# Kernel optimization log

Measured on AMD Instinct MI355X. Metric: run time of the kernel, lower is better.

The kernel has to match this reference:

```python
import jax, jax.numpy as jnp
import numpy as np

B, N, E = 16, 2048, 1024
G, V = 2, 320
D = E // G
TAU = 2.0


def setup_inputs() -> dict:
    key = jax.random.key(0)
    k1, k2, k3, k4 = jax.random.split(key, 4)
    x = jax.random.normal(k1, (B, N, E), dtype=jnp.float32)
    u = jax.random.uniform(k2, (B, N, G, V), dtype=jnp.float32)
    W = jax.random.normal(k3, (E, G * V), dtype=jnp.float32) * 0.02
    b = jnp.zeros((G * V,), dtype=jnp.float32)
    codebook = jax.random.normal(k4, (G, V, D), dtype=jnp.float32)
    return {"x": x, "u": u, "W": W, "b": b, "codebook": codebook}


def reference(x, u, W, b, codebook):
    Bx, Nx, Ex = x.shape
    Gx, Vx, Dx = codebook.shape
    # linear projection -> per-group logits [B,N,G,V]
    h = (jnp.einsum('bne,ef->bnf', x, W) + b).reshape(Bx, Nx, Gx, Vx)
    # gumbel noise from uniform samples (clamped away from 0/1)
    eps = 1e-7
    g = -jnp.log(-jnp.log(u * (1.0 - 2.0 * eps) + eps))
    soft = jax.nn.softmax((h + g) / TAU, axis=-1)
    # hard one-hot with straight-through estimator (matches torch hard=True)
    idx = jnp.argmax(soft, axis=-1)
    hard = jax.nn.one_hot(idx, Vx, dtype=soft.dtype)
    y = hard - jax.lax.stop_gradient(soft) + soft  # [B,N,G,V]
    # select code vectors: equivalent to broadcast-mul + sum over V
    code_vector = jnp.einsum('bngv,gvd->bngd', y, codebook).reshape(Bx, Nx, Gx * Dx)
    # codebook usage entropy: sum one-hots over time, softmax over V per group
    p = jax.nn.softmax(jnp.sum(y, axis=1), axis=-1)  # [B,G,V]
    entropy = -jnp.sum(p * jnp.log(p + 1e-8)) / (Gx * Vx)
    return code_vector, entropy
```

## Files before the change

kernel.cpp:

```cpp
#include <hip/hip_runtime.h>

namespace {

constexpr int Bsz = 16, Nsz = 2048, Esz = 1024, Gsz = 2, Vsz = 320, Dsz = 512;
constexpr int Msz = Bsz * Nsz;
constexpr int Fsz = Gsz * Vsz;
constexpr int BM = 128, BN = 128, BK = 32;
constexpr int NKC = Esz / 32;
constexpr int NMB = Msz / 16;
constexpr int NFB = Fsz / 16;

typedef __attribute__((ext_vector_type(8))) short bf16x8;
typedef __attribute__((ext_vector_type(4))) float f32x4;
typedef unsigned int u32;
typedef unsigned short u16;

__device__ __forceinline__ void load_lds16(const void* g, void* l) {
  __builtin_amdgcn_global_load_lds(
      (const __attribute__((address_space(1))) u32*)g,
      (__attribute__((address_space(3))) u32*)l, 16, 0, 0);
}

__device__ __forceinline__ ushort f2bf(float f) {
  union { float f; unsigned u; } v; v.f = f;
  unsigned r = (v.u + 0x7FFFu + ((v.u >> 16) & 1u)) >> 16;
  return (ushort)r;
}
__device__ __forceinline__ float bf2f(ushort h) {
  union { unsigned u; float f; } v; v.u = ((unsigned)h) << 16;
  return v.f;
}

__device__ __forceinline__ float gumb_precise(float uu) {
  const float C0 = 1.0f - 2.0f * 1e-7f;
  float up = uu * C0;
  up = up + 1e-7f;
  return -logf(-logf(up));
}
__device__ __forceinline__ float gumb_fast(float uu) {
  const float C0 = 1.0f - 2.0f * 1e-7f;
  const float up = fmaf(uu, C0, 1e-7f);
  const float d = 1.0f - up;
  const float ypoly =
      d * fmaf(d, fmaf(d, fmaf(d, fmaf(d, 0.2f, 0.25f), 0.33333334f), 0.5f), 1.0f);
  const float yfast = -__logf(up);
  const float y = (up >= 0.84f) ? ypoly : yfast;
  return -__logf(y);
}

struct Top2 { float v1, v2; int i1, i2; };
__device__ __forceinline__ void t2_feed(Top2& t, float z, int f) {
  if (z > t.v1 || (z == t.v1 && f < t.i1)) {
    t.v2 = t.v1; t.i2 = t.i1; t.v1 = z; t.i1 = f;
  } else if (z > t.v2 || (z == t.v2 && f < t.i2)) {
    t.v2 = z; t.i2 = f;
  }
}
__device__ __forceinline__ void t2_merge(Top2& t, float ov1, int oi1, float ov2,
                                         int oi2) {
  if (ov1 > t.v1 || (ov1 == t.v1 && oi1 < t.i1)) {
    const bool keep = (t.v1 > ov2) || (t.v1 == ov2 && t.i1 < oi2);
    t.v2 = keep ? t.v1 : ov2; t.i2 = keep ? t.i1 : oi2;
    t.v1 = ov1; t.i1 = oi1;
  } else if (ov1 > t.v2 || (ov1 == t.v2 && oi1 < t.i2)) {
    t.v2 = ov1; t.i2 = oi1;
  }
}

__device__ __forceinline__ uint2 pack_hi_trunc(float4 a) {
  uint2 r;
  r.x = (__float_as_uint(a.x) >> 16) | (__float_as_uint(a.y) & 0xffff0000u);
  r.y = (__float_as_uint(a.z) >> 16) | (__float_as_uint(a.w) & 0xffff0000u);
  return r;
}
__device__ __forceinline__ float4 resid_trunc(float4 a) {
  float4 r;
  r.x = a.x - __uint_as_float(__float_as_uint(a.x) & 0xffff0000u);
  r.y = a.y - __uint_as_float(__float_as_uint(a.y) & 0xffff0000u);
  r.z = a.z - __uint_as_float(__float_as_uint(a.z) & 0xffff0000u);
  r.w = a.w - __uint_as_float(__float_as_uint(a.w) & 0xffff0000u);
  return r;
}


__global__ __launch_bounds__(256) void k_prep(const float* __restrict__ W,
                                              u16* __restrict__ wt,
                                              float* __restrict__ wtT) {
  const int tid = threadIdx.x;
  const int l = tid & 63;
  const int blob = blockIdx.x * 4 + (tid >> 6);
  const int fb = blob >> 5, kc = blob & 31;
  const int f = fb * 16 + (l & 15);
  const int k0 = kc * 32 + (l >> 4) * 8;
  float v[8];
  ushort hh[8], ll[8];
#pragma unroll
  for (int j = 0; j < 8; ++j) {
    v[j] = W[(size_t)(k0 + j) * Fsz + f];
    hh[j] = f2bf(v[j]);
    ll[j] = f2bf(v[j] - bf2f(hh[j]));
  }
  uint4 qh, ql;
  qh.x = hh[0] | ((u32)hh[1] << 16); qh.y = hh[2] | ((u32)hh[3] << 16);
  qh.z = hh[4] | ((u32)hh[5] << 16); qh.w = hh[6] | ((u32)hh[7] << 16);
  ql.x = ll[0] | ((u32)ll[1] << 16); ql.y = ll[2] | ((u32)ll[3] << 16);
  ql.z = ll[4] | ((u32)ll[5] << 16); ql.w = ll[6] | ((u32)ll[7] << 16);
  const size_t b2 = (size_t)(kc * NFB + fb);
  *(uint4*)(wt + (b2 * 2 + 0) * 512 + l * 8) = qh;
  *(uint4*)(wt + (b2 * 2 + 1) * 512 + l * 8) = ql;
  float4 t0, t1;
  t0.x = v[0]; t0.y = v[1]; t0.z = v[2]; t0.w = v[3];
  t1.x = v[4]; t1.y = v[5]; t1.z = v[6]; t1.w = v[7];
  *(float4*)(wtT + (size_t)f * Esz + k0) = t0;
  *(float4*)(wtT + (size_t)f * Esz + k0 + 4) = t1;
}

__global__ __launch_bounds__(256) void k_prepx(const float* __restrict__ x,
                                               u16* __restrict__ xt) {
  const int tid = threadIdx.x;
  const int l = tid & 63;
  const int blob = blockIdx.x * 4 + (tid >> 6);
  const int mb = blob >> 5, kc = blob & 31;
  const size_t row = (size_t)mb * 16 + (l & 15);
  const int k0 = kc * 32 + (l >> 4) * 8;
  const float4 a0 = *(const float4*)(x + row * Esz + k0);
  const float4 a1 = *(const float4*)(x + row * Esz + k0 + 4);
  const uint2 h0 = pack_hi_trunc(a0), h1 = pack_hi_trunc(a1);
  const uint2 l0 = pack_hi_trunc(resid_trunc(a0));
  const uint2 l1 = pack_hi_trunc(resid_trunc(a1));
  uint4 qh, ql;
  qh.x = h0.x; qh.y = h0.y; qh.z = h1.x; qh.w = h1.y;
  ql.x = l0.x; ql.y = l0.y; ql.z = l1.x; ql.w = l1.y;
  const size_t b2 = (size_t)kc * NMB + mb;
  *(uint4*)(xt + (b2 * 2 + 0) * 512 + l * 8) = qh;
  *(uint4*)(xt + (b2 * 2 + 1) * 512 + l * 8) = ql;
}

__global__ __launch_bounds__(256, 4) void k_gemm(
    const float* __restrict__ u, const float* __restrict__ bias,
    const u16* __restrict__ xt, const u16* __restrict__ wt,
    float4* __restrict__ partial) {
  __shared__ __align__(16) u16 sm[8192];

  const int tid = threadIdx.x;
  const int bid = blockIdx.x;
  const int tile = (bid & 7) * 320 + (bid >> 3);
  const int mt = tile / 10, nt = tile - mt * 10;
  const int m0 = mt * BM;
  const int n0 = nt * 64;

  const int lane = tid & 63, w = tid >> 6;
  const int lrow = lane & 15, quad = lane >> 4;

  f32x4 acc[2][4];
#pragma unroll
  for (int i = 0; i < 2; ++i)
#pragma unroll
    for (int j = 0; j < 4; ++j) acc[i][j] = (f32x4){0.f, 0.f, 0.f, 0.f};

  const size_t KSTEP_A = (size_t)NMB * 1024;
  const size_t KSTEP_B = (size_t)NFB * 1024;
  const u16* abase = xt + (size_t)(m0 >> 4) * 1024 + lane * 8;
  const u16* wbase = wt + (size_t)(n0 >> 4) * 1024 + lane * 8;

  auto stageA = [&](int kc) {
    const u16* s = abase + (size_t)kc * KSTEP_A;
#pragma unroll
    for (int i = 0; i < 4; ++i) {
      const int cc = w + 4 * i;
      load_lds16(s + cc * 512, sm + cc * 512);
    }
  };

  bf16x8 bh[4], bl[4];
  auto loadB = [&](int kc) {
    const u16* s = wbase + (size_t)kc * KSTEP_B;
#pragma unroll
    for (int ct = 0; ct < 4; ++ct) {
      bh[ct] = *(const bf16x8*)(s + ct * 1024);
      bl[ct] = *(const bf16x8*)(s + ct * 1024 + 512);
    }
  };

  stageA(0);
  loadB(0);

  for (int kc = 0; kc < NKC; ++kc) {
    __syncthreads();
    bf16x8 ah[2], al[2];
#pragma unroll
    for (int rt = 0; rt < 2; ++rt) {
      const int blk = w * 2 + rt;
      ah[rt] = *(const bf16x8*)(sm + (blk * 2 + 0) * 512 + lane * 8);
      al[rt] = *(const bf16x8*)(sm + (blk * 2 + 1) * 512 + lane * 8);
    }
    __syncthreads();
    if (kc + 1 < NKC) stageA(kc + 1);
    __builtin_amdgcn_sched_barrier(0);
    __builtin_amdgcn_s_setprio(1);
#pragma unroll
    for (int ct = 0; ct < 4; ++ct)
#pragma unroll
      for (int rt = 0; rt < 2; ++rt) {
        acc[rt][ct] = __builtin_amdgcn_mfma_f32_16x16x32_bf16(al[rt], bh[ct], acc[rt][ct], 0, 0, 0);
        acc[rt][ct] = __builtin_amdgcn_mfma_f32_16x16x32_bf16(ah[rt], bl[ct], acc[rt][ct], 0, 0, 0);
        acc[rt][ct] = __builtin_amdgcn_mfma_f32_16x16x32_bf16(ah[rt], bh[ct], acc[rt][ct], 0, 0, 0);
      }
    __builtin_amdgcn_s_setprio(0);
    if (kc + 1 < NKC) loadB(kc + 1);
  }

  const int pcol = nt;
#pragma unroll
  for (int rt = 0; rt < 2; ++rt) {
#pragma unroll
    for (int rg = 0; rg < 4; ++rg) {
      const int row = w * 32 + rt * 16 + quad * 4 + rg;
      const size_t m = (size_t)(m0 + row);
      Top2 t; t.v1 = -3.4e38f; t.v2 = -3.4e38f; t.i1 = 1 << 30; t.i2 = 1 << 30;
#pragma unroll
      for (int ct = 0; ct < 4; ++ct) {
        const int f = n0 + ct * 16 + lrow;
        const float z = acc[rt][ct][rg] + bias[f] + gumb_fast(u[m * 640 + f]);
        t2_feed(t, z, f);
      }
#pragma unroll
      for (int off = 1; off < 16; off <<= 1) {
        const float ov1 = __shfl_xor(t.v1, off, 16);
        const int oi1 = __shfl_xor(t.i1, off, 16);
        const float ov2 = __shfl_xor(t.v2, off, 16);
        const int oi2 = __shfl_xor(t.i2, off, 16);
        t2_merge(t, ov1, oi1, ov2, oi2);
      }
      if (lrow == 0) {
        float4 o;
        o.x = t.v1; o.y = __int_as_float(t.i1);
        o.z = t.v2; o.w = __int_as_float(t.i2);
        partial[m * 10 + pcol] = o;
      }
    }
  }
}

__global__ __launch_bounds__(256) void k_select(
    const float4* __restrict__ partial, const float* __restrict__ x,
    const float* __restrict__ wtT, const float* __restrict__ bias,
    const float* __restrict__ u, int2* __restrict__ idx_out,
    int* __restrict__ counts) {
  const int tid = threadIdx.x;
  const size_t m = (size_t)blockIdx.x * 256 + tid;
  int vsel[2];
#pragma unroll
  for (int g = 0; g < 2; ++g) {
    Top2 t; t.v1 = -3.4e38f; t.v2 = -3.4e38f; t.i1 = 1 << 30; t.i2 = 1 << 30;
#pragma unroll
    for (int p = 0; p < 5; ++p) {
      const float4 q = partial[m * 10 + g * 5 + p];
      t2_merge(t, q.x, __float_as_int(q.y), q.z, __float_as_int(q.w));
    }
    int i1 = t.i1;
    if (t.v1 - t.v2 < 1e-3f) {
      const int i2 = t.i2;
      const float* xp = x + m * Esz;
      const float* w1 = wtT + (size_t)i1 * Esz;
      const float* w2 = wtT + (size_t)i2 * Esz;
      float h1 = 0.f, h2 = 0.f;
      for (int k = 0; k < Esz; k += 4) {
        const float4 xv = *(const float4*)(xp + k);
        const float4 a = *(const float4*)(w1 + k);
        const float4 b = *(const float4*)(w2 + k);
        h1 = fmaf(xv.x, a.x, h1); h1 = fmaf(xv.y, a.y, h1);
        h1 = fmaf(xv.z, a.z, h1); h1 = fmaf(xv.w, a.w, h1);
        h2 = fmaf(xv.x, b.x, h2); h2 = fmaf(xv.y, b.y, h2);
        h2 = fmaf(xv.z, b.z, h2); h2 = fmaf(xv.w, b.w, h2);
      }
      const float z1 = h1 + bias[i1] + gumb_precise(u[m * 640 + i1]);
      const float z2 = h2 + bias[i2] + gumb_precise(u[m * 640 + i2]);
      if (z2 > z1 || (z2 == z1 && i2 < i1)) i1 = i2;
    }
    const int v = i1 - g * Vsz;
    vsel[g] = v;
    const int b = (int)(m >> 11);
    atomicAdd(&counts[(b * Gsz + g) * Vsz + v], 1);
  }
  int2 r; r.x = vsel[0]; r.y = vsel[1];
  idx_out[m] = r;
}

__global__ __launch_bounds__(256) void k_gather(const int2* __restrict__ idx,
                                                const float* __restrict__ cb,
                                                float* __restrict__ out) {
  const int tid = threadIdx.x;
  const size_t mbase = (size_t)blockIdx.x * 8;
  const int gq = tid >> 7, dq = tid & 127;
#pragma unroll
  for (int it = 0; it < 8; ++it) {
    const int2 p = idx[mbase + it];
    const int v = gq ? p.y : p.x;
    const float4 cv =
        *(const float4*)(cb + ((size_t)(gq * Vsz + v)) * Dsz + dq * 4);
    *(float4*)(out + (mbase + it) * (size_t)(Gsz * Dsz) + tid * 4) = cv;
  }
}


__global__ __launch_bounds__(256) void k_prep_fb(const float* __restrict__ W,
                                                 u16* __restrict__ wt_h,
                                                 u16* __restrict__ wt_l) {
  const int f = blockIdx.x;
  const int k0 = threadIdx.x * 4;
  float v[4];
#pragma unroll
  for (int i = 0; i < 4; ++i) v[i] = W[(size_t)(k0 + i) * Fsz + f];
  ushort4 hh, ll;
  hh.x = f2bf(v[0]); ll.x = f2bf(v[0] - bf2f(hh.x));
  hh.y = f2bf(v[1]); ll.y = f2bf(v[1] - bf2f(hh.y));
  hh.z = f2bf(v[2]); ll.z = f2bf(v[2] - bf2f(hh.z));
  hh.w = f2bf(v[3]); ll.w = f2bf(v[3] - bf2f(hh.w));
  *(ushort4*)(wt_h + (size_t)f * Esz + k0) = hh;
  *(ushort4*)(wt_l + (size_t)f * Esz + k0) = ll;
}

__global__ __launch_bounds__(256) void k_gemm_fb(
    const float* __restrict__ x, const float* __restrict__ u,
    const float* __restrict__ bias, const u16* __restrict__ wth,
    const u16* __restrict__ wtl, float4* __restrict__ partial) {
  __shared__ __align__(16) u16 sm[16384];
  u16* xs_h = sm;
  u16* xs_l = sm + 4096;
  u16* bs_h = sm + 8192;
  u16* bs_l = sm + 12288;

  const int tid = threadIdx.x;
  const int n0 = blockIdx.x * BN;
  const int m0 = blockIdx.y * BM;
  const int lane = tid & 63, w = tid >> 6;
  const int wr = w >> 1, wc = w & 1;
  const int lrow = lane & 15, quad = lane >> 4;

  f32x4 acc[4][4];
#pragma unroll
  for (int i = 0; i < 4; ++i)
#pragma unroll
    for (int j = 0; j < 4; ++j) acc[i][j] = (f32x4){0.f, 0.f, 0.f, 0.f};

  for (int k0 = 0; k0 < Esz; k0 += BK) {
    float4 av[4];
#pragma unroll
    for (int s = 0; s < 4; ++s) {
      const int id = tid + 256 * s;
      const int row = id >> 3, kq = id & 7;
      av[s] = *(const float4*)(x + (size_t)(m0 + row) * Esz + k0 + kq * 4);
    }
    __syncthreads();
#pragma unroll
    for (int c = 0; c < 4; ++c) {
      const int chunk = w + 4 * c;
      const int plane = chunk >> 3, ch = chunk & 7;
      const u16* src = (plane ? wtl : wth) +
                       (size_t)(n0 + ch * 16 + (lane >> 2)) * Esz + k0 +
                       (lane & 3) * 8;
      u16* dst = (plane ? bs_l : bs_h) + ch * 512;
      load_lds16(src, dst);
    }
#pragma unroll
    for (int s = 0; s < 4; ++s) {
      const int id = tid + 256 * s;
      const int row = id >> 3, kq = id & 7;
      const u32 u0 = __float_as_uint(av[s].x), u1 = __float_as_uint(av[s].y);
      const u32 u2 = __float_as_uint(av[s].z), u3 = __float_as_uint(av[s].w);
      uint2 hh, ll;
      hh.x = (u0 >> 16) | (u1 & 0xffff0000u);
      hh.y = (u2 >> 16) | (u3 & 0xffff0000u);
      const float r0 = av[s].x - __uint_as_float(u0 & 0xffff0000u);
      const float r1 = av[s].y - __uint_as_float(u1 & 0xffff0000u);
      const float r2 = av[s].z - __uint_as_float(u2 & 0xffff0000u);
      const float r3 = av[s].w - __uint_as_float(u3 & 0xffff0000u);
      ll.x = (__float_as_uint(r0) >> 16) | (__float_as_uint(r1) & 0xffff0000u);
      ll.y = (__float_as_uint(r2) >> 16) | (__float_as_uint(r3) & 0xffff0000u);
      *(uint2*)(xs_h + row * 32 + kq * 4) = hh;
      *(uint2*)(xs_l + row * 32 + kq * 4) = ll;
    }
    __syncthreads();

    bf16x8 ah[4], al[4];
#pragma unroll
    for (int rt = 0; rt < 4; ++rt) {
      const int off = (wr * 64 + rt * 16 + lrow) * 32 + quad * 8;
      ah[rt] = *(const bf16x8*)(xs_h + off);
      al[rt] = *(const bf16x8*)(xs_l + off);
    }
#pragma unroll
    for (int ct = 0; ct < 4; ++ct) {
      const int off = (wc * 64 + ct * 16 + lrow) * 32 + quad * 8;
      const bf16x8 bh = *(const bf16x8*)(bs_h + off);
      const bf16x8 bl = *(const bf16x8*)(bs_l + off);
#pragma unroll
      for (int rt = 0; rt < 4; ++rt) {
        acc[rt][ct] = __builtin_amdgcn_mfma_f32_16x16x32_bf16(al[rt], bh, acc[rt][ct], 0, 0, 0);
        acc[rt][ct] = __builtin_amdgcn_mfma_f32_16x16x32_bf16(ah[rt], bl, acc[rt][ct], 0, 0, 0);
        acc[rt][ct] = __builtin_amdgcn_mfma_f32_16x16x32_bf16(ah[rt], bh, acc[rt][ct], 0, 0, 0);
      }
    }
  }

  const int pcol = blockIdx.x * 2 + wc;
#pragma unroll
  for (int rt = 0; rt < 4; ++rt) {
#pragma unroll
    for (int rg = 0; rg < 4; ++rg) {
      const int row = wr * 64 + rt * 16 + quad * 4 + rg;
      const size_t m = (size_t)(m0 + row);
      Top2 t; t.v1 = -3.4e38f; t.v2 = -3.4e38f; t.i1 = 1 << 30; t.i2 = 1 << 30;
#pragma unroll
      for (int ct = 0; ct < 4; ++ct) {
        const int f = n0 + wc * 64 + ct * 16 + lrow;
        const float z = acc[rt][ct][rg] + bias[f] + gumb_fast(u[m * 640 + f]);
        t2_feed(t, z, f);
      }
#pragma unroll
      for (int off = 1; off < 16; off <<= 1) {
        const float ov1 = __shfl_xor(t.v1, off, 16);
        const int oi1 = __shfl_xor(t.i1, off, 16);
        const float ov2 = __shfl_xor(t.v2, off, 16);
        const int oi2 = __shfl_xor(t.i2, off, 16);
        t2_merge(t, ov1, oi1, ov2, oi2);
      }
      if (lrow == 0) {
        float4 o;
        o.x = t.v1; o.y = __int_as_float(t.i1);
        o.z = t.v2; o.w = __int_as_float(t.i2);
        partial[m * 10 + pcol] = o;
      }
    }
  }
}

__global__ __launch_bounds__(256) void k_select_fb(
    const float4* __restrict__ partial, const float* __restrict__ x,
    const float* __restrict__ W, const float* __restrict__ bias,
    const float* __restrict__ u, const float* __restrict__ cb,
    float* __restrict__ out, int* __restrict__ counts) {
  __shared__ int idx_sh[256][2];
  const int tid = threadIdx.x;
  const size_t m = (size_t)blockIdx.x * 256 + tid;

#pragma unroll
  for (int g = 0; g < 2; ++g) {
    Top2 t; t.v1 = -3.4e38f; t.v2 = -3.4e38f; t.i1 = 1 << 30; t.i2 = 1 << 30;
#pragma unroll
    for (int p = 0; p < 5; ++p) {
      const float4 q = partial[m * 10 + g * 5 + p];
      t2_merge(t, q.x, __float_as_int(q.y), q.z, __float_as_int(q.w));
    }
    int i1 = t.i1;
    if (t.v1 - t.v2 < 1e-3f) {
      const int i2 = t.i2;
      const float* xp = x + m * Esz;
      float h1 = 0.f, h2 = 0.f;
      for (int k = 0; k < Esz; ++k) {
        const float xv = xp[k];
        h1 = fmaf(xv, W[(size_t)k * Fsz + i1], h1);
        h2 = fmaf(xv, W[(size_t)k * Fsz + i2], h2);
      }
      const float z1 = h1 + bias[i1] + gumb_precise(u[m * 640 + i1]);
      const float z2 = h2 + bias[i2] + gumb_precise(u[m * 640 + i2]);
      if (z2 > z1 || (z2 == z1 && i2 < i1)) i1 = i2;
    }
    const int v = i1 - g * Vsz;
    idx_sh[tid][g] = v;
    const int b = (int)(m >> 11);
    atomicAdd(&counts[(b * Gsz + g) * Vsz + v], 1);
  }
  __syncthreads();

  const size_t mbase = (size_t)blockIdx.x * 256;
  const int gq = tid >> 7, dq = tid & 127;
  for (int it = 0; it < 256; ++it) {
    const int v = idx_sh[it][gq];
    const float4 cv =
        *(const float4*)(cb + ((size_t)(gq * Vsz + v)) * Dsz + dq * 4);
    *(float4*)(out + (mbase + it) * (size_t)(Gsz * Dsz) + tid * 4) = cv;
  }
}

__global__ __launch_bounds__(64) void k_entropy(const int* __restrict__ counts,
                                                float* __restrict__ partial) {
  const int bg = blockIdx.x;
  const int lane = threadIdx.x;
  float c[5];
  float mx = -3.4e38f;
#pragma unroll
  for (int t = 0; t < 5; ++t) {
    c[t] = (float)counts[bg * Vsz + lane + 64 * t];
    mx = fmaxf(mx, c[t]);
  }
#pragma unroll
  for (int off = 32; off; off >>= 1) mx = fmaxf(mx, __shfl_xor(mx, off));
  float e[5];
  float s = 0.f;
#pragma unroll
  for (int t = 0; t < 5; ++t) {
    e[t] = expf(c[t] - mx);
    s += e[t];
  }
#pragma unroll
  for (int off = 32; off; off >>= 1) s += __shfl_xor(s, off);
  float ent = 0.f;
#pragma unroll
  for (int t = 0; t < 5; ++t) {
    const float p = e[t] / s;
    ent += p * logf(p + 1e-8f);
  }
#pragma unroll
  for (int off = 32; off; off >>= 1) ent += __shfl_xor(ent, off);
  if (lane == 0) partial[bg] = ent;
}

__global__ __launch_bounds__(64) void k_final(const float* __restrict__ partial,
                                              float* __restrict__ dst) {
  const int lane = threadIdx.x;
  float v = (lane < 32) ? partial[lane] : 0.f;
#pragma unroll
  for (int off = 32; off; off >>= 1) v += __shfl_xor(v, off);
  if (lane == 0) dst[0] = -v / (float)(Gsz * Vsz);
}

}

extern "C" void kernel_launch(void* const* d_in, const int* in_sizes, int n_in,
                              void* d_out, int out_size, void* d_ws,
                              size_t ws_size, hipStream_t stream) {
  const float* x = (const float*)d_in[0];
  const float* u = (const float*)d_in[1];
  const float* W = (const float*)d_in[2];
  const float* bias = (const float*)d_in[3];
  const float* cb = (const float*)d_in[4];
  float* out = (float*)d_out;

  int* counts = (int*)d_ws;
  float* epart = (float*)((char*)d_ws + 40960);
  float4* partial = (float4*)((char*)d_ws + 65536);
  const size_t PART_END = 65536 + (size_t)Msz * 10 * 16;
  const size_t NEED_NEW =
      PART_END + 262144 + 2621440 + 2621440 + (size_t)Msz * Esz * 4;

  hipMemsetAsync(d_ws, 0, 40960, stream);

  if (ws_size >= NEED_NEW) {
    int2* idx = (int2*)((char*)d_ws + PART_END);
    u16* wt = (u16*)((char*)d_ws + PART_END + 262144);
    float* wtT = (float*)((char*)d_ws + PART_END + 262144 + 2621440);
    u16* xt = (u16*)((char*)d_ws + PART_END + 262144 + 2621440 + 2621440);
    k_prep<<<320, 256, 0, stream>>>(W, wt, wtT);
    k_prepx<<<16384, 256, 0, stream>>>(x, xt);
    k_gemm<<<(Msz / BM) * 10, 256, 0, stream>>>(u, bias, xt, wt, partial);
    k_select<<<Msz / 256, 256, 0, stream>>>(partial, x, wtT, bias, u, idx,
                                            counts);
    k_gather<<<Msz / 8, 256, 0, stream>>>(idx, cb, out);
  } else {
    u16* wth = (u16*)((char*)d_ws + PART_END);
    u16* wtl = wth + (size_t)Fsz * Esz;
    k_prep_fb<<<Fsz, 256, 0, stream>>>(W, wth, wtl);
    k_gemm_fb<<<dim3(Fsz / BN, Msz / BM), 256, 0, stream>>>(x, u, bias, wth,
                                                            wtl, partial);
    k_select_fb<<<Msz / 256, 256, 0, stream>>>(partial, x, W, bias, u, cb, out,
                                               counts);
  }
  k_entropy<<<Bsz * Gsz, 64, 0, stream>>>(counts, epart);
  k_final<<<1, 64, 0, stream>>>(epart, out + (size_t)Msz * Esz);
}
```

Baseline: 549.8 us.

## Swap GEMM staging: A via registers, B via double-buffered LDS

The GEMM main loop stops staging the A tile (x) through LDS and instead prefetches each wave's private A rows straight into registers with two alternating register sets. The shared B tile (W) now goes into LDS with a double buffer, so the next k-chunk loads while the current one feeds the MFMAs. The loop is unrolled by two, and each iteration still has two barriers. This is meant to hide global latency better and to put shared operands in LDS, at the cost of more VGPRs, which could lower occupancy.

Result: faster. 512.5 us (-6.8%).

```diff
diff --git a/kernel.cpp b/kernel.cpp
--- a/kernel.cpp
+++ b/kernel.cpp
@@ -160,55 +160,84 @@
 
   const size_t KSTEP_A = (size_t)NMB * 1024;
   const size_t KSTEP_B = (size_t)NFB * 1024;
-  const u16* abase = xt + (size_t)(m0 >> 4) * 1024 + lane * 8;
+  const u16* abase = xt + (size_t)((m0 >> 4) + w * 2) * 1024 + lane * 8;
   const u16* wbase = wt + (size_t)(n0 >> 4) * 1024 + lane * 8;
 
-  auto stageA = [&](int kc) {
-    const u16* s = abase + (size_t)kc * KSTEP_A;
-#pragma unroll
-    for (int i = 0; i < 4; ++i) {
+  auto stageB = [&](int kc, int buf) {
+    const u16* s = wbase + (size_t)kc * KSTEP_B;
+#pragma unroll
+    for (int i = 0; i < 2; ++i) {
       const int cc = w + 4 * i;
-      load_lds16(s + cc * 512, sm + cc * 512);
+      load_lds16(s + cc * 512, sm + buf * 4096 + cc * 512);
     }
   };
 
+  bf16x8 a0h0, a0h1, a0l0, a0l1;
+  bf16x8 a1h0, a1h1, a1l0, a1l1;
+
+#define PREF_A0(kc)                                            \
+  {                                                            \
+    const u16* s_ = abase + (size_t)(kc) * KSTEP_A;            \
+    a0h0 = *(const bf16x8*)(s_);                               \
+    a0l0 = *(const bf16x8*)(s_ + 512);                         \
+    a0h1 = *(const bf16x8*)(s_ + 1024);                        \
+    a0l1 = *(const bf16x8*)(s_ + 1536);                        \
+  }
+#define PREF_A1(kc)                                            \
+  {                                                            \
+    const u16* s_ = abase + (size_t)(kc) * KSTEP_A;            \
+    a1h0 = *(const bf16x8*)(s_);                               \
+    a1l0 = *(const bf16x8*)(s_ + 512);                         \
+    a1h1 = *(const bf16x8*)(s_ + 1024);                        \
+    a1l1 = *(const bf16x8*)(s_ + 1536);                        \
+  }
+
   bf16x8 bh[4], bl[4];
-  auto loadB = [&](int kc) {
-    const u16* s = wbase + (size_t)kc * KSTEP_B;
+  auto readB = [&](int buf) {
+    const u16* base = sm + buf * 4096 + lane * 8;
 #pragma unroll
     for (int ct = 0; ct < 4; ++ct) {
-      bh[ct] = *(const bf16x8*)(s + ct * 1024);
-      bl[ct] = *(const bf16x8*)(s + ct * 1024 + 512);
+      bh[ct] = *(const bf16x8*)(base + ct * 1024);
+      bl[ct] = *(const bf16x8*)(base + ct * 1024 + 512);
     }
   };
 
-  stageA(0);
-  loadB(0);
-
-  for (int kc = 0; kc < NKC; ++kc) {
+#define MFMA_CLUSTER(AH0, AL0, AH1, AL1)                                       \
+  __builtin_amdgcn_s_setprio(1);                                               \
+  _Pragma("unroll")                                                            \
+  for (int ct = 0; ct < 4; ++ct) {                                             \
+    acc[0][ct] = __builtin_amdgcn_mfma_f32_16x16x32_bf16(AL0, bh[ct], acc[0][ct], 0, 0, 0); \
+    acc[0][ct] = __builtin_amdgcn_mfma_f32_16x16x32_bf16(AH0, bl[ct], acc[0][ct], 0, 0, 0); \
+    acc[0][ct] = __builtin_amdgcn_mfma_f32_16x16x32_bf16(AH0, bh[ct], acc[0][ct], 0, 0, 0); \
+    acc[1][ct] = __builtin_amdgcn_mfma_f32_16x16x32_bf16(AL1, bh[ct], acc[1][ct], 0, 0, 0); \
+    acc[1][ct] = __builtin_amdgcn_mfma_f32_16x16x32_bf16(AH1, bl[ct], acc[1][ct], 0, 0, 0); \
+    acc[1][ct] = __builtin_amdgcn_mfma_f32_16x16x32_bf16(AH1, bh[ct], acc[1][ct], 0, 0, 0); \
+  }                                                                            \
+  __builtin_amdgcn_s_setprio(0);
+
+  PREF_A0(0);
+  stageB(0, 0);
+
+  for (int it = 0; it < NKC / 2; ++it) {
+    const int kc = it * 2;
     __syncthreads();
-    bf16x8 ah[2], al[2];
-#pragma unroll
-    for (int rt = 0; rt < 2; ++rt) {
-      const int blk = w * 2 + rt;
-      ah[rt] = *(const bf16x8*)(sm + (blk * 2 + 0) * 512 + lane * 8);
-      al[rt] = *(const bf16x8*)(sm + (blk * 2 + 1) * 512 + lane * 8);
-    }
+    stageB(kc + 1, 1);
+    PREF_A1(kc + 1);
+    __builtin_amdgcn_sched_barrier(0);
+    readB(0);
+    MFMA_CLUSTER(a0h0, a0l0, a0h1, a0l1);
     __syncthreads();
-    if (kc + 1 < NKC) stageA(kc + 1);
+    if (kc + 2 < NKC) {
+      stageB(kc + 2, 0);
+      PREF_A0(kc + 2);
+    }
     __builtin_amdgcn_sched_barrier(0);
-    __builtin_amdgcn_s_setprio(1);
-#pragma unroll
-    for (int ct = 0; ct < 4; ++ct)
-#pragma unroll
-      for (int rt = 0; rt < 2; ++rt) {
-        acc[rt][ct] = __builtin_amdgcn_mfma_f32_16x16x32_bf16(al[rt], bh[ct], acc[rt][ct], 0, 0, 0);
-        acc[rt][ct] = __builtin_amdgcn_mfma_f32_16x16x32_bf16(ah[rt], bl[ct], acc[rt][ct], 0, 0, 0);
-        acc[rt][ct] = __builtin_amdgcn_mfma_f32_16x16x32_bf16(ah[rt], bh[ct], acc[rt][ct], 0, 0, 0);
-      }
-    __builtin_amdgcn_s_setprio(0);
-    if (kc + 1 < NKC) loadB(kc + 1);
-  }
+    readB(1);
+    MFMA_CLUSTER(a1h0, a1l0, a1h1, a1l1);
+  }
+#undef PREF_A0
+#undef PREF_A1
+#undef MFMA_CLUSTER
 
   const int pcol = nt;
 #pragma unroll
```
